# Kernel optimization log

Measured on AMD Instinct MI355X. Metric: run time of the kernel, lower is better.

Reference implementation:

```python
import jax, jax.numpy as jnp
import numpy as np

DROPOUT_RATE = 0.5
CONF_THRESH = 0.85
IGNORE_VALUE = 2
EPS = 1e-07


def setup_inputs() -> dict:
    key = jax.random.key(0)
    k1, k2 = jax.random.split(key)
    B, H, W = 16, 1024, 1024
    pred = jax.random.uniform(k1, (B, H, W), dtype=jnp.float32)
    mask = jax.random.randint(k2, (B, H, W), 0, 3, dtype=jnp.int32)
    return {"pred": pred, "mask": mask}


def _training_need_score(pred, gt, confidence):
    # Higher = needs more training: CW=4, UW=3, UC=2, CC=1 (+/- confidence bonus)
    is_correct = (pred > 0.5) == (gt == 1.0)
    is_conf = confidence > CONF_THRESH
    score = jnp.where(is_conf & is_correct, 1.0,
            jnp.where(~is_conf & is_correct, 2.0,
            jnp.where(~is_conf & ~is_correct, 3.0, 4.0))).astype(pred.dtype)
    bonus = (confidence - 0.5) * 0.5
    return jnp.where(is_correct, score - bonus, score + bonus)


def _dynamic_masks(pred, mask):
    # Vectorized equivalent of the per-batch nonzero/argsort/scatter loop:
    # rank annotated pixels per batch by descending need-score; top n_train -> train.
    B, H, W = mask.shape
    annotated = (mask != IGNORE_VALUE).reshape(B, H * W)
    gt = mask.astype(pred.dtype)
    confidence = jnp.maximum(pred, 1.0 - pred)
    scores = _training_need_score(pred, gt, confidence).reshape(B, H * W)
    neg_inf = jnp.asarray(-jnp.inf, scores.dtype)
    masked_scores = jnp.where(annotated, scores, neg_inf)
    order = jnp.argsort(-masked_scores, axis=1)          # descending score order
    rank = jnp.argsort(order, axis=1)                    # rank of each pixel in that order
    n_points = annotated.sum(axis=1)
    n_train = (n_points.astype(jnp.float32) * (1.0 - DROPOUT_RATE)).astype(jnp.int32)
    train = annotated & (rank < n_train[:, None])
    holdout = annotated & ~train
    return train.reshape(B, H, W), holdout.reshape(B, H, W)


def reference(pred, mask):
    if pred.ndim == 4 and pred.shape[1] == 1:
        pred = pred[:, 0]
    train_mask, holdout_mask = _dynamic_masks(pred, mask)
    gt = mask.astype(pred.dtype)
    p = jnp.clip(pred, EPS, 1.0 - EPS)
    bce = -(gt * jnp.log(p) + (1.0 - gt) * jnp.log(1.0 - p))
    tm = train_mask.astype(pred.dtype)
    loss = (bce * tm).sum() / (tm.sum() + EPS)
    return loss, train_mask, holdout_mask
```

## Files before the change

kernel.cpp:

```cpp
#include <hip/hip_runtime.h>
#include <stdint.h>

#define NBATCH 16
#define HW_ (1 << 20)
#define TPB 256

#define NBPB_H 32
#define TPB_H 512
#define EPB_H (HW_ / NBPB_H)
#define ITER_H (EPB_H / (TPB_H * 4))

#define NBINS 8192
#define FBASE 0x3F400

#define NBPB_F 256
#define FCHUNK (HW_ / NBPB_F)

#define CAND_CAP 32768
#define LCAP 512
#define TIE_CAP 4096
#define CNT_STRIDE 64

typedef float f4v __attribute__((ext_vector_type(4)));

struct BParams {
    unsigned int k;
    unsigned int bin1f;
    unsigned int r;
    unsigned int mode;
};

__device__ __forceinline__ unsigned int score_bits(float p, int m) {
    bool correct = (p > 0.5f) == (m == 1);
    float conf = fmaxf(p, 1.0f - p);
    float base = correct ? ((conf > 0.85f) ? 1.0f : 2.0f)
                         : ((conf > 0.85f) ? 4.0f : 3.0f);
    float bonus = (conf - 0.5f) * 0.5f;
    float s = correct ? (base - bonus) : (base + bonus);
    return __float_as_uint(s);
}

__global__ void k_hist1(const float4* __restrict__ pred4, const int4* __restrict__ mask4,
                        unsigned int* __restrict__ hist1) {
    __shared__ unsigned int lh[NBINS];
    int b = blockIdx.x / NBPB_H;
    int blk = blockIdx.x % NBPB_H;
    for (int i = threadIdx.x; i < NBINS; i += TPB_H) lh[i] = 0;
    __syncthreads();
    int l4base = blk * (EPB_H / 4);
    for (int j = 0; j < ITER_H; j++) {
        int i4l = l4base + j * TPB_H + threadIdx.x;
        size_t g4 = (size_t)b * (HW_ / 4) + i4l;
        float4 p = pred4[g4];
        int4 m = mask4[g4];
        float pa[4] = {p.x, p.y, p.z, p.w};
        int ma[4] = {m.x, m.y, m.z, m.w};
#pragma unroll
        for (int l = 0; l < 4; l++) {
            if (ma[l] != 2) {
                unsigned int sb = score_bits(pa[l], ma[l]);
                int fb = (int)(sb >> 12) - FBASE;
                fb = min(max(fb, 0), NBINS - 1);
                atomicAdd(&lh[fb], 1u);
            }
        }
    }
    __syncthreads();
    for (int i = threadIdx.x; i < NBINS; i += TPB_H)
        if (lh[i]) atomicAdd(&hist1[b * NBINS + i], lh[i]);
}

__global__ void k_find1(const unsigned int* __restrict__ hist1, BParams* prm) {
    int b = blockIdx.x;
    int t = threadIdx.x;
    __shared__ unsigned int cs_[257];
    const unsigned int* h = hist1 + (size_t)b * NBINS;
    {
        const uint4* h4 = (const uint4*)(h + t * 32);
        unsigned int s = 0;
#pragma unroll
        for (int j = 0; j < 8; j++) { uint4 v = h4[j]; s += v.x + v.y + v.z + v.w; }
        cs_[t] = s;
        if (t == 0) cs_[256] = 0;
    }
    __syncthreads();
    for (int off = 1; off < 256; off <<= 1) {
        unsigned int a = (t + off < 256) ? cs_[t + off] : 0u;
        __syncthreads();
        cs_[t] += a;
        __syncthreads();
    }
    unsigned int n = cs_[0];
    unsigned int k = (unsigned int)(int)((float)n * 0.5f);
    if (k == 0) {
        if (t == 0) {
            BParams P;
            P.k = 0; P.bin1f = 0xFFFFFFFFu; P.r = 0; P.mode = 0;
            prm[b] = P;
        }
        return;
    }
    if (cs_[t] >= k && cs_[t + 1] < k) {
        unsigned int cum = cs_[t + 1];
        for (int j = 31; j >= 0; j--) {
            unsigned int hb = h[t * 32 + j];
            if (cum + hb >= k) {
                BParams P;
                P.k = k;
                P.bin1f = (unsigned int)(FBASE + t * 32 + j);
                P.r = k - cum;
                P.mode = 1;
                prm[b] = P;
                break;
            }
            cum += hb;
        }
    }
}

__global__ void k_main(const float4* __restrict__ pred4, const int4* __restrict__ mask4,
                       const BParams* __restrict__ prm, float* __restrict__ out,
                       float* __restrict__ partials, unsigned int* __restrict__ cand_cnt,
                       unsigned int* __restrict__ cand_idx, unsigned int* __restrict__ cand_sb,
                       float* __restrict__ cand_bce) {
    int b = blockIdx.x / NBPB_F;
    int blk = blockIdx.x % NBPB_F;
    BParams P = prm[b];
    unsigned int target = P.bin1f;
    __shared__ unsigned int lcode[FCHUNK / 4];
    __shared__ float red[TPB];
    __shared__ unsigned int l_idx[LCAP];
    __shared__ unsigned int l_sb[LCAP];
    __shared__ float l_bce[LCAP];
    __shared__ unsigned int lcnt;
    __shared__ unsigned int gbase;
    if (threadIdx.x == 0) lcnt = 0;
    __syncthreads();
    float acc = 0.0f;
    int ibase = blk * FCHUNK;
    for (int j = 0; j < FCHUNK / (TPB * 4); j++) {
        int v = j * TPB + threadIdx.x;
        size_t g4 = (size_t)b * (HW_ / 4) + (ibase / 4) + v;
        float4 p = pred4[g4];
        int4 m = mask4[g4];
        float pa[4] = {p.x, p.y, p.z, p.w};
        int ma[4] = {m.x, m.y, m.z, m.w};
        unsigned int cw = 0;
#pragma unroll
        for (int l = 0; l < 4; l++) {
            bool ann = (ma[l] != 2);
            unsigned int sb = score_bits(pa[l], ma[l]);
            unsigned int fine = sb >> 12;
            bool tr = ann && (fine > target);
            bool amb = ann && (fine == target);
            unsigned int code = (tr ? 1u : 0u) | ((ann && !tr) ? 2u : 0u);
            cw |= code << (8 * l);
            float bce = 0.0f;
            if (tr || amb) {
                float pc = fminf(fmaxf(pa[l], 1e-7f), 1.0f - 1e-7f);
                bce = (ma[l] == 1) ? -__logf(pc) : -__logf(1.0f - pc);
            }
            if (tr) acc += bce;
            if (amb) {
                unsigned int p0 = atomicAdd(&lcnt, 1u);
                if (p0 < LCAP) {
                    l_idx[p0] = (unsigned int)(ibase + v * 4 + l);
                    l_sb[p0] = sb;
                    l_bce[p0] = bce;
                } else {
                    unsigned int gp = atomicAdd(&cand_cnt[b * CNT_STRIDE], 1u);
                    if (gp < CAND_CAP) {
                        size_t o = (size_t)b * CAND_CAP + gp;
                        cand_idx[o] = (unsigned int)(ibase + v * 4 + l);
                        cand_sb[o] = sb;
                        cand_bce[o] = bce;
                    }
                }
            }
        }
        lcode[v] = cw;
    }
    __syncthreads();
    unsigned int n = min(lcnt, (unsigned int)LCAP);
    if (threadIdx.x == 0 && n > 0)
        gbase = atomicAdd(&cand_cnt[b * CNT_STRIDE], n);
    __syncthreads();
    for (unsigned int i = threadIdx.x; i < n; i += TPB) {
        unsigned int pos = gbase + i;
        if (pos < CAND_CAP) {
            size_t o = (size_t)b * CAND_CAP + pos;
            cand_idx[o] = l_idx[i];
            cand_sb[o] = l_sb[i];
            cand_bce[o] = l_bce[i];
        }
    }
    float* trout = out + 1;
    float* hoout = out + 1 + (size_t)NBATCH * HW_;
    size_t Gbase = (size_t)b * HW_ + (size_t)ibase;
    for (int v = threadIdx.x; v < FCHUNK / 4 - 1; v += TPB) {
        unsigned int w0 = lcode[v];
        unsigned int w1 = lcode[v + 1];
        unsigned int c0 = (w0 >> 24) & 0xFFu;
        unsigned int c1 = w1 & 0xFFu;
        unsigned int c2 = (w1 >> 8) & 0xFFu;
        unsigned int c3 = (w1 >> 16) & 0xFFu;
        int e = 3 + 4 * v;
        f4v tv = { (float)(c0 & 1u), (float)(c1 & 1u), (float)(c2 & 1u), (float)(c3 & 1u) };
        f4v hv = { (float)((c0 >> 1) & 1u), (float)((c1 >> 1) & 1u),
                   (float)((c2 >> 1) & 1u), (float)((c3 >> 1) & 1u) };
        __builtin_nontemporal_store(tv, (f4v*)(trout + Gbase + e));
        __builtin_nontemporal_store(hv, (f4v*)(hoout + Gbase + e));
    }
    if (threadIdx.x < 3) {
        unsigned int c = (lcode[0] >> (8 * threadIdx.x)) & 0xFFu;
        trout[Gbase + threadIdx.x] = (float)(c & 1u);
        hoout[Gbase + threadIdx.x] = (float)((c >> 1) & 1u);
    }
    if (threadIdx.x == 3) {
        unsigned int c = (lcode[FCHUNK / 4 - 1] >> 24) & 0xFFu;
        trout[Gbase + FCHUNK - 1] = (float)(c & 1u);
        hoout[Gbase + FCHUNK - 1] = (float)((c >> 1) & 1u);
    }
    red[threadIdx.x] = acc;
    __syncthreads();
    for (int off = TPB / 2; off > 0; off >>= 1) {
        if (threadIdx.x < off) red[threadIdx.x] += red[threadIdx.x + off];
        __syncthreads();
    }
    if (threadIdx.x == 0) partials[blockIdx.x] = red[0];
}

__global__ void k_fixup(const unsigned int* __restrict__ cand_cnt,
                        const unsigned int* __restrict__ cand_idx,
                        const unsigned int* __restrict__ cand_sb,
                        const float* __restrict__ cand_bce,
                        const BParams* __restrict__ prm, float* __restrict__ out,
                        float* __restrict__ tie_partials) {
    int b = blockIdx.x;
    int t = threadIdx.x;
    __shared__ unsigned int h[4096];
    __shared__ unsigned int cs_[257];
    __shared__ unsigned int tie_idx[TIE_CAP];
    __shared__ unsigned int misc[8];
    __shared__ float red[TPB];
    BParams P = prm[b];
    if (P.mode == 0) {
        if (t == 0) tie_partials[b] = 0.0f;
        return;
    }
    unsigned int C = cand_cnt[b * CNT_STRIDE];
    if (C > CAND_CAP) C = CAND_CAP;
    const unsigned int* ci = cand_idx + (size_t)b * CAND_CAP;
    const unsigned int* cs = cand_sb + (size_t)b * CAND_CAP;
    const float* cb = cand_bce + (size_t)b * CAND_CAP;
    for (int i = t; i < 4096; i += TPB) h[i] = 0;
    if (t < 8) misc[t] = (t == 4) ? 0xFFFFFFFFu : 0u;
    __syncthreads();
    for (unsigned int i = t; i < C; i += TPB)
        atomicAdd(&h[cs[i] & 0xFFFu], 1u);
    __syncthreads();
    {
        unsigned int gs = 0;
#pragma unroll
        for (int j = 0; j < 16; j++) gs += h[t * 16 + j];
        cs_[t] = gs;
        if (t == 0) cs_[256] = 0;
    }
    __syncthreads();
    for (int off = 1; off < 256; off <<= 1) {
        unsigned int a = (t + off < 256) ? cs_[t + off] : 0u;
        __syncthreads();
        cs_[t] += a;
        __syncthreads();
    }
    if (cs_[t] >= P.r && cs_[t + 1] < P.r) {
        unsigned int cum = cs_[t + 1];
        for (int j = 15; j >= 0; j--) {
            unsigned int hb = h[t * 16 + j];
            if (cum + hb >= P.r) {
                unsigned int T = P.r - cum;
                misc[0] = (unsigned int)(t * 16 + j);
                misc[1] = T;
                misc[2] = (T == hb) ? 1u : 0u;
                break;
            }
            cum += hb;
        }
    }
    __syncthreads();
    unsigned int vstar = misc[0], T = misc[1];
    bool allTies = (misc[2] != 0);
    unsigned int idxcut;
    if (allTies) {
        idxcut = 0xFFFFFFFFu;
    } else {
        for (unsigned int i = t; i < C; i += TPB) {
            if ((cs[i] & 0xFFFu) == vstar) {
                unsigned int p = atomicAdd(&misc[3], 1u);
                if (p < TIE_CAP) tie_idx[p] = ci[i];
            }
        }
        __syncthreads();
        unsigned int E2 = misc[3];
        if (E2 > TIE_CAP) E2 = TIE_CAP;
        for (unsigned int i = t; i < E2; i += TPB) {
            unsigned int vi = tie_idx[i];
            unsigned int cnt = 0;
            for (unsigned int j = 0; j < E2; j++) cnt += (tie_idx[j] < vi) ? 1u : 0u;
            if (cnt == T - 1) misc[4] = vi;
        }
        __syncthreads();
        idxcut = misc[4];
    }
    float acc = 0.0f;
    float* trout = out + 1;
    float* hoout = out + 1 + (size_t)NBATCH * HW_;
    size_t base = (size_t)b * HW_;
    for (unsigned int i = t; i < C; i += TPB) {
        unsigned int low = cs[i] & 0xFFFu;
        bool tr = (low > vstar) || (low == vstar && ci[i] <= idxcut);
        if (tr) {
            trout[base + ci[i]] = 1.0f;
            hoout[base + ci[i]] = 0.0f;
            acc += cb[i];
        }
    }
    red[t] = acc;
    __syncthreads();
    for (int off = TPB / 2; off > 0; off >>= 1) {
        if (t < off) red[t] += red[t + off];
        __syncthreads();
    }
    if (t == 0) tie_partials[b] = red[0];
}

__global__ void k_loss(const float* __restrict__ partials, const float* __restrict__ tie_partials,
                       const BParams* __restrict__ prm, float* __restrict__ out) {
    __shared__ double red[TPB];
    double s = 0.0;
    for (int i = threadIdx.x; i < NBATCH * NBPB_F; i += TPB) s += (double)partials[i];
    if (threadIdx.x < NBATCH) s += (double)tie_partials[threadIdx.x];
    red[threadIdx.x] = s;
    __syncthreads();
    for (int off = TPB / 2; off > 0; off >>= 1) {
        if (threadIdx.x < off) red[threadIdx.x] += red[threadIdx.x + off];
        __syncthreads();
    }
    if (threadIdx.x == 0) {
        unsigned long long den = 0;
        for (int b = 0; b < NBATCH; b++) den += prm[b].k;
        float denf = (float)den + 1e-7f;
        out[0] = (float)red[0] / denf;
    }
}

extern "C" void kernel_launch(void* const* d_in, const int* in_sizes, int n_in,
                              void* d_out, int out_size, void* d_ws, size_t ws_size,
                              hipStream_t stream) {
    const float4* pred4 = (const float4*)d_in[0];
    const int4* mask4 = (const int4*)d_in[1];
    float* out = (float*)d_out;

    unsigned int* hist1 = (unsigned int*)d_ws;
    unsigned int* cand_cnt = hist1 + NBATCH * NBINS;
    BParams* prm = (BParams*)(cand_cnt + NBATCH * CNT_STRIDE);
    float* partials = (float*)(prm + NBATCH);
    float* tie_partials = partials + NBATCH * NBPB_F;
    unsigned int* cand_idx = (unsigned int*)(tie_partials + NBATCH);
    unsigned int* cand_sb = cand_idx + NBATCH * CAND_CAP;
    float* cand_bce = (float*)(cand_sb + NBATCH * CAND_CAP);

    size_t zero_bytes = (size_t)(NBATCH * NBINS + NBATCH * CNT_STRIDE) * 4;
    hipMemsetAsync(d_ws, 0, zero_bytes, stream);

    k_hist1<<<dim3(NBATCH * NBPB_H), dim3(TPB_H), 0, stream>>>(pred4, mask4, hist1);
    k_find1<<<dim3(NBATCH), dim3(TPB), 0, stream>>>(hist1, prm);
    k_main<<<dim3(NBATCH * NBPB_F), dim3(TPB), 0, stream>>>(pred4, mask4, prm, out, partials,
                                                            cand_cnt, cand_idx, cand_sb, cand_bce);
    k_fixup<<<dim3(NBATCH), dim3(TPB), 0, stream>>>(cand_cnt, cand_idx, cand_sb, cand_bce,
                                                    prm, out, tie_partials);
    k_loss<<<dim3(1), dim3(TPB), 0, stream>>>(partials, tie_partials, prm, out);
}
```

Before: 284.2 us.

## Fuse all five stages into one cooperative persistent kernel with grid syncs

Replaces the histogram, threshold-find, main, fixup and loss kernels with a single cooperative kernel of 1024 blocks that separates the stages with grid.sync(), reusing one shared-memory union across phases. Each block handles the same input chunk in both the histogram and main passes, which may give L2 reuse of pred/mask on the second read, and it removes four kernel launch gaps. The cost is grid-wide barriers, one fixed block count (occupancy limited by a 32KB histogram per block plus the union), and serial phases where only 16 blocks work while the rest wait. TIE_CAP is also reduced.

```diff
diff --git a/kernel.cpp b/kernel.cpp
--- a/kernel.cpp
+++ b/kernel.cpp
@@ -1,24 +1,24 @@
 #include <hip/hip_runtime.h>
+#include <hip/hip_cooperative_groups.h>
 #include <stdint.h>
+
+namespace cg = cooperative_groups;
 
 #define NBATCH 16
 #define HW_ (1 << 20)
 #define TPB 256
-
-#define NBPB_H 32
-#define TPB_H 512
-#define EPB_H (HW_ / NBPB_H)
-#define ITER_H (EPB_H / (TPB_H * 4))
+#define NBLOCKS 1024
+#define BPB (NBLOCKS / NBATCH)
+#define EPB (HW_ / BPB)
+#define E4PB (EPB / 4)
+#define ITERS (E4PB / TPB)
 
 #define NBINS 8192
 #define FBASE 0x3F400
 
-#define NBPB_F 256
-#define FCHUNK (HW_ / NBPB_F)
-
 #define CAND_CAP 32768
 #define LCAP 512
-#define TIE_CAP 4096
+#define TIE_CAP 1024
 #define CNT_STRIDE 64
 
 typedef float f4v __attribute__((ext_vector_type(4)));
@@ -29,6 +29,22 @@
     unsigned int r;
     unsigned int mode;
 };
+
+struct SP1 { unsigned int hist[NBINS]; };
+struct SP2 { unsigned int cs_[257]; };
+struct SP3 {
+    unsigned int lcode[E4PB];
+    unsigned int l_idx[LCAP]; unsigned int l_sb[LCAP]; float l_bce[LCAP];
+    float red[TPB];
+    unsigned int lcnt, gbase;
+};
+struct SP4 {
+    unsigned int h[4096]; unsigned int cs_[257];
+    unsigned int tie_idx[TIE_CAP]; unsigned int misc[8];
+    float red[TPB];
+};
+struct SP5 { double red[TPB]; };
+union SmemU { SP1 p1; SP2 p2; SP3 p3; SP4 p4; SP5 p5; };
 
 __device__ __forceinline__ unsigned int score_bits(float p, int m) {
     bool correct = (p > 0.5f) == (m == 1);
@@ -40,19 +56,29 @@
     return __float_as_uint(s);
 }
 
-__global__ void k_hist1(const float4* __restrict__ pred4, const int4* __restrict__ mask4,
-                        unsigned int* __restrict__ hist1) {
-    __shared__ unsigned int lh[NBINS];
-    int b = blockIdx.x / NBPB_H;
-    int blk = blockIdx.x % NBPB_H;
-    for (int i = threadIdx.x; i < NBINS; i += TPB_H) lh[i] = 0;
+__global__ __launch_bounds__(TPB, 4) void k_all(
+    const float4* __restrict__ pred4, const int4* __restrict__ mask4,
+    float* __restrict__ out,
+    unsigned int* __restrict__ hist1, unsigned int* __restrict__ cand_cnt,
+    BParams* __restrict__ prm, float* __restrict__ partials,
+    float* __restrict__ tie_partials,
+    unsigned int* __restrict__ cand_idx, unsigned int* __restrict__ cand_sb,
+    float* __restrict__ cand_bce)
+{
+    cg::grid_group grid = cg::this_grid();
+    __shared__ SmemU sm;
+    const int b = blockIdx.x / BPB;
+    const int blk = blockIdx.x % BPB;
+    const int t = threadIdx.x;
+    const size_t batch4 = (size_t)b * (HW_ / 4);
+    const int l4base = blk * E4PB;
+
+    for (int i = t; i < NBINS; i += TPB) sm.p1.hist[i] = 0;
     __syncthreads();
-    int l4base = blk * (EPB_H / 4);
-    for (int j = 0; j < ITER_H; j++) {
-        int i4l = l4base + j * TPB_H + threadIdx.x;
-        size_t g4 = (size_t)b * (HW_ / 4) + i4l;
-        float4 p = pred4[g4];
-        int4 m = mask4[g4];
+    for (int j = 0; j < ITERS; j++) {
+        int i4 = l4base + j * TPB + t;
+        float4 p = pred4[batch4 + i4];
+        int4 m = mask4[batch4 + i4];
         float pa[4] = {p.x, p.y, p.z, p.w};
         int ma[4] = {m.x, m.y, m.z, m.w};
 #pragma unroll
@@ -61,296 +87,268 @@
                 unsigned int sb = score_bits(pa[l], ma[l]);
                 int fb = (int)(sb >> 12) - FBASE;
                 fb = min(max(fb, 0), NBINS - 1);
-                atomicAdd(&lh[fb], 1u);
+                atomicAdd(&sm.p1.hist[fb], 1u);
             }
         }
     }
     __syncthreads();
-    for (int i = threadIdx.x; i < NBINS; i += TPB_H)
-        if (lh[i]) atomicAdd(&hist1[b * NBINS + i], lh[i]);
-}
-
-__global__ void k_find1(const unsigned int* __restrict__ hist1, BParams* prm) {
-    int b = blockIdx.x;
-    int t = threadIdx.x;
-    __shared__ unsigned int cs_[257];
-    const unsigned int* h = hist1 + (size_t)b * NBINS;
+    for (int i = t; i < NBINS; i += TPB) {
+        unsigned int v = sm.p1.hist[i];
+        if (v) atomicAdd(&hist1[b * NBINS + i], v);
+    }
+    grid.sync();
+
+    if (blockIdx.x < NBATCH) {
+        int bb = blockIdx.x;
+        const unsigned int* h = hist1 + (size_t)bb * NBINS;
+        {
+            const uint4* h4 = (const uint4*)(h + t * 32);
+            unsigned int s = 0;
+#pragma unroll
+            for (int j = 0; j < 8; j++) { uint4 v = h4[j]; s += v.x + v.y + v.z + v.w; }
+            sm.p2.cs_[t] = s;
+            if (t == 0) sm.p2.cs_[256] = 0;
+        }
+        __syncthreads();
+        for (int off = 1; off < 256; off <<= 1) {
+            unsigned int a = (t + off < 256) ? sm.p2.cs_[t + off] : 0u;
+            __syncthreads();
+            sm.p2.cs_[t] += a;
+            __syncthreads();
+        }
+        unsigned int n = sm.p2.cs_[0];
+        unsigned int k = (unsigned int)(int)((float)n * 0.5f);
+        if (k == 0) {
+            if (t == 0) {
+                BParams P; P.k = 0; P.bin1f = 0xFFFFFFFFu; P.r = 0; P.mode = 0;
+                prm[bb] = P;
+            }
+        } else if (sm.p2.cs_[t] >= k && sm.p2.cs_[t + 1] < k) {
+            unsigned int cum = sm.p2.cs_[t + 1];
+            for (int j = 31; j >= 0; j--) {
+                unsigned int hb = h[t * 32 + j];
+                if (cum + hb >= k) {
+                    BParams P;
+                    P.k = k; P.bin1f = (unsigned int)(FBASE + t * 32 + j);
+                    P.r = k - cum; P.mode = 1;
+                    prm[bb] = P;
+                    break;
+                }
+                cum += hb;
+            }
+        }
+    }
+    grid.sync();
+
     {
-        const uint4* h4 = (const uint4*)(h + t * 32);
-        unsigned int s = 0;
+        BParams P = prm[b];
+        unsigned int target = P.bin1f;
+        if (t == 0) sm.p3.lcnt = 0;
+        __syncthreads();
+        float acc = 0.0f;
+        for (int j = 0; j < ITERS; j++) {
+            int v = j * TPB + t;
+            float4 p = pred4[batch4 + l4base + v];
+            int4 m = mask4[batch4 + l4base + v];
+            float pa[4] = {p.x, p.y, p.z, p.w};
+            int ma[4] = {m.x, m.y, m.z, m.w};
+            unsigned int cw = 0;
 #pragma unroll
-        for (int j = 0; j < 8; j++) { uint4 v = h4[j]; s += v.x + v.y + v.z + v.w; }
-        cs_[t] = s;
-        if (t == 0) cs_[256] = 0;
-    }
-    __syncthreads();
-    for (int off = 1; off < 256; off <<= 1) {
-        unsigned int a = (t + off < 256) ? cs_[t + off] : 0u;
-        __syncthreads();
-        cs_[t] += a;
-        __syncthreads();
-    }
-    unsigned int n = cs_[0];
-    unsigned int k = (unsigned int)(int)((float)n * 0.5f);
-    if (k == 0) {
+            for (int l = 0; l < 4; l++) {
+                bool ann = (ma[l] != 2);
+                unsigned int sb = score_bits(pa[l], ma[l]);
+                unsigned int fine = sb >> 12;
+                bool tr = ann && (fine > target);
+                bool amb = ann && (fine == target);
+                unsigned int code = (tr ? 1u : 0u) | ((ann && !tr) ? 2u : 0u);
+                cw |= code << (8 * l);
+                float bce = 0.0f;
+                if (tr || amb) {
+                    float pc = fminf(fmaxf(pa[l], 1e-7f), 1.0f - 1e-7f);
+                    bce = (ma[l] == 1) ? -__logf(pc) : -__logf(1.0f - pc);
+                }
+                if (tr) acc += bce;
+                if (amb) {
+                    unsigned int p0 = atomicAdd(&sm.p3.lcnt, 1u);
+                    if (p0 < LCAP) {
+                        sm.p3.l_idx[p0] = (unsigned int)(blk * EPB + v * 4 + l);
+                        sm.p3.l_sb[p0] = sb;
+                        sm.p3.l_bce[p0] = bce;
+                    } else {
+                        unsigned int gp = atomicAdd(&cand_cnt[b * CNT_STRIDE], 1u);
+                        if (gp < CAND_CAP) {
+                            size_t o = (size_t)b * CAND_CAP + gp;
+                            cand_idx[o] = (unsigned int)(blk * EPB + v * 4 + l);
+                            cand_sb[o] = sb;
+                            cand_bce[o] = bce;
+                        }
+                    }
+                }
+            }
+            sm.p3.lcode[v] = cw;
+        }
+        __syncthreads();
+        unsigned int n = min(sm.p3.lcnt, (unsigned int)LCAP);
+        if (t == 0 && n > 0)
+            sm.p3.gbase = atomicAdd(&cand_cnt[b * CNT_STRIDE], n);
+        __syncthreads();
+        for (unsigned int i = t; i < n; i += TPB) {
+            unsigned int pos = sm.p3.gbase + i;
+            if (pos < CAND_CAP) {
+                size_t o = (size_t)b * CAND_CAP + pos;
+                cand_idx[o] = sm.p3.l_idx[i];
+                cand_sb[o] = sm.p3.l_sb[i];
+                cand_bce[o] = sm.p3.l_bce[i];
+            }
+        }
+        float* trout = out + 1;
+        float* hoout = out + 1 + (size_t)NBATCH * HW_;
+        size_t Gbase = (size_t)b * HW_ + (size_t)blk * EPB;
+        for (int v = t; v < E4PB - 1; v += TPB) {
+            unsigned int w0 = sm.p3.lcode[v];
+            unsigned int w1 = sm.p3.lcode[v + 1];
+            unsigned int c0 = (w0 >> 24) & 0xFFu;
+            unsigned int c1 = w1 & 0xFFu;
+            unsigned int c2 = (w1 >> 8) & 0xFFu;
+            unsigned int c3 = (w1 >> 16) & 0xFFu;
+            int e = 3 + 4 * v;
+            f4v tv = { (float)(c0 & 1u), (float)(c1 & 1u), (float)(c2 & 1u), (float)(c3 & 1u) };
+            f4v hv = { (float)((c0 >> 1) & 1u), (float)((c1 >> 1) & 1u),
+                       (float)((c2 >> 1) & 1u), (float)((c3 >> 1) & 1u) };
+            __builtin_nontemporal_store(tv, (f4v*)(trout + Gbase + e));
+            __builtin_nontemporal_store(hv, (f4v*)(hoout + Gbase + e));
+        }
+        if (t < 3) {
+            unsigned int c = (sm.p3.lcode[0] >> (8 * t)) & 0xFFu;
+            trout[Gbase + t] = (float)(c & 1u);
+            hoout[Gbase + t] = (float)((c >> 1) & 1u);
+        }
+        if (t == 3) {
+            unsigned int c = (sm.p3.lcode[E4PB - 1] >> 24) & 0xFFu;
+            trout[Gbase + EPB - 1] = (float)(c & 1u);
+            hoout[Gbase + EPB - 1] = (float)((c >> 1) & 1u);
+        }
+        sm.p3.red[t] = acc;
+        __syncthreads();
+        for (int off = TPB / 2; off > 0; off >>= 1) {
+            if (t < off) sm.p3.red[t] += sm.p3.red[t + off];
+            __syncthreads();
+        }
+        if (t == 0) partials[blockIdx.x] = sm.p3.red[0];
+    }
+    grid.sync();
+
+    if (blockIdx.x < NBATCH) {
+        int bb = blockIdx.x;
+        BParams P = prm[bb];
+        if (P.mode == 0) {
+            if (t == 0) tie_partials[bb] = 0.0f;
+        } else {
+            unsigned int C = cand_cnt[bb * CNT_STRIDE];
+            if (C > CAND_CAP) C = CAND_CAP;
+            const unsigned int* ci = cand_idx + (size_t)bb * CAND_CAP;
+            const unsigned int* cs = cand_sb + (size_t)bb * CAND_CAP;
+            const float* cb = cand_bce + (size_t)bb * CAND_CAP;
+            for (int i = t; i < 4096; i += TPB) sm.p4.h[i] = 0;
+            if (t < 8) sm.p4.misc[t] = (t == 4) ? 0xFFFFFFFFu : 0u;
+            __syncthreads();
+            for (unsigned int i = t; i < C; i += TPB)
+                atomicAdd(&sm.p4.h[cs[i] & 0xFFFu], 1u);
+            __syncthreads();
+            {
+                unsigned int gs = 0;
+#pragma unroll
+                for (int j = 0; j < 16; j++) gs += sm.p4.h[t * 16 + j];
+                sm.p4.cs_[t] = gs;
+                if (t == 0) sm.p4.cs_[256] = 0;
+            }
+            __syncthreads();
+            for (int off = 1; off < 256; off <<= 1) {
+                unsigned int a = (t + off < 256) ? sm.p4.cs_[t + off] : 0u;
+                __syncthreads();
+                sm.p4.cs_[t] += a;
+                __syncthreads();
+            }
+            if (sm.p4.cs_[t] >= P.r && sm.p4.cs_[t + 1] < P.r) {
+                unsigned int cum = sm.p4.cs_[t + 1];
+                for (int j = 15; j >= 0; j--) {
+                    unsigned int hb = sm.p4.h[t * 16 + j];
+                    if (cum + hb >= P.r) {
+                        unsigned int T = P.r - cum;
+                        sm.p4.misc[0] = (unsigned int)(t * 16 + j);
+                        sm.p4.misc[1] = T;
+                        sm.p4.misc[2] = (T == hb) ? 1u : 0u;
+                        break;
+                    }
+                    cum += hb;
+                }
+            }
+            __syncthreads();
+            unsigned int vstar = sm.p4.misc[0], T = sm.p4.misc[1];
+            bool allTies = (sm.p4.misc[2] != 0);
+            unsigned int idxcut;
+            if (allTies) {
+                idxcut = 0xFFFFFFFFu;
+            } else {
+                for (unsigned int i = t; i < C; i += TPB) {
+                    if ((cs[i] & 0xFFFu) == vstar) {
+                        unsigned int p = atomicAdd(&sm.p4.misc[3], 1u);
+                        if (p < TIE_CAP) sm.p4.tie_idx[p] = ci[i];
+                    }
+                }
+                __syncthreads();
+                unsigned int E2 = sm.p4.misc[3];
+                if (E2 > TIE_CAP) E2 = TIE_CAP;
+                for (unsigned int i = t; i < E2; i += TPB) {
+                    unsigned int vi = sm.p4.tie_idx[i];
+                    unsigned int cnt = 0;
+                    for (unsigned int j = 0; j < E2; j++)
+                        cnt += (sm.p4.tie_idx[j] < vi) ? 1u : 0u;
+                    if (cnt == T - 1) sm.p4.misc[4] = vi;
+                }
+                __syncthreads();
+                idxcut = sm.p4.misc[4];
+            }
+            float acc = 0.0f;
+            float* trout = out + 1;
+            float* hoout = out + 1 + (size_t)NBATCH * HW_;
+            size_t base = (size_t)bb * HW_;
+            for (unsigned int i = t; i < C; i += TPB) {
+                unsigned int low = cs[i] & 0xFFFu;
+                bool tr = (low > vstar) || (low == vstar && ci[i] <= idxcut);
+                if (tr) {
+                    trout[base + ci[i]] = 1.0f;
+                    hoout[base + ci[i]] = 0.0f;
+                    acc += cb[i];
+                }
+            }
+            sm.p4.red[t] = acc;
+            __syncthreads();
+            for (int off = TPB / 2; off > 0; off >>= 1) {
+                if (t < off) sm.p4.red[t] += sm.p4.red[t + off];
+                __syncthreads();
+            }
+            if (t == 0) tie_partials[bb] = sm.p4.red[0];
+        }
+    }
+    grid.sync();
+
+    if (blockIdx.x == 0) {
+        double s = 0.0;
+        for (int i = t; i < NBLOCKS; i += TPB) s += (double)partials[i];
+        if (t < NBATCH) s += (double)tie_partials[t];
+        sm.p5.red[t] = s;
+        __syncthreads();
+        for (int off = TPB / 2; off > 0; off >>= 1) {
+            if (t < off) sm.p5.red[t] += sm.p5.red[t + off];
+            __syncthreads();
+        }
         if (t == 0) {
-            BParams P;
-            P.k = 0; P.bin1f = 0xFFFFFFFFu; P.r = 0; P.mode = 0;
-            prm[b] = P;
-        }
-        return;
-    }
-    if (cs_[t] >= k && cs_[t + 1] < k) {
-        unsigned int cum = cs_[t + 1];
-        for (int j = 31; j >= 0; j--) {
-            unsigned int hb = h[t * 32 + j];
-            if (cum + hb >= k) {
-                BParams P;
-                P.k = k;
-                P.bin1f = (unsigned int)(FBASE + t * 32 + j);
-                P.r = k - cum;
-                P.mode = 1;
-                prm[b] = P;
-                break;
-            }
-            cum += hb;
-        }
-    }
-}
-
-__global__ void k_main(const float4* __restrict__ pred4, const int4* __restrict__ mask4,
-                       const BParams* __restrict__ prm, float* __restrict__ out,
-                       float* __restrict__ partials, unsigned int* __restrict__ cand_cnt,
-                       unsigned int* __restrict__ cand_idx, unsigned int* __restrict__ cand_sb,
-                       float* __restrict__ cand_bce) {
-    int b = blockIdx.x / NBPB_F;
-    int blk = blockIdx.x % NBPB_F;
-    BParams P = prm[b];
-    unsigned int target = P.bin1f;
-    __shared__ unsigned int lcode[FCHUNK / 4];
-    __shared__ float red[TPB];
-    __shared__ unsigned int l_idx[LCAP];
-    __shared__ unsigned int l_sb[LCAP];
-    __shared__ float l_bce[LCAP];
-    __shared__ unsigned int lcnt;
-    __shared__ unsigned int gbase;
-    if (threadIdx.x == 0) lcnt = 0;
-    __syncthreads();
-    float acc = 0.0f;
-    int ibase = blk * FCHUNK;
-    for (int j = 0; j < FCHUNK / (TPB * 4); j++) {
-        int v = j * TPB + threadIdx.x;
-        size_t g4 = (size_t)b * (HW_ / 4) + (ibase / 4) + v;
-        float4 p = pred4[g4];
-        int4 m = mask4[g4];
-        float pa[4] = {p.x, p.y, p.z, p.w};
-        int ma[4] = {m.x, m.y, m.z, m.w};
-        unsigned int cw = 0;
-#pragma unroll
-        for (int l = 0; l < 4; l++) {
-            bool ann = (ma[l] != 2);
-            unsigned int sb = score_bits(pa[l], ma[l]);
-            unsigned int fine = sb >> 12;
-            bool tr = ann && (fine > target);
-            bool amb = ann && (fine == target);
-            unsigned int code = (tr ? 1u : 0u) | ((ann && !tr) ? 2u : 0u);
-            cw |= code << (8 * l);
-            float bce = 0.0f;
-            if (tr || amb) {
-                float pc = fminf(fmaxf(pa[l], 1e-7f), 1.0f - 1e-7f);
-                bce = (ma[l] == 1) ? -__logf(pc) : -__logf(1.0f - pc);
-            }
-            if (tr) acc += bce;
-            if (amb) {
-                unsigned int p0 = atomicAdd(&lcnt, 1u);
-                if (p0 < LCAP) {
-                    l_idx[p0] = (unsigned int)(ibase + v * 4 + l);
-                    l_sb[p0] = sb;
-                    l_bce[p0] = bce;
-                } else {
-                    unsigned int gp = atomicAdd(&cand_cnt[b * CNT_STRIDE], 1u);
-                    if (gp < CAND_CAP) {
-                        size_t o = (size_t)b * CAND_CAP + gp;
-                        cand_idx[o] = (unsigned int)(ibase + v * 4 + l);
-                        cand_sb[o] = sb;
-                        cand_bce[o] = bce;
-                    }
-                }
-            }
-        }
-        lcode[v] = cw;
-    }
-    __syncthreads();
-    unsigned int n = min(lcnt, (unsigned int)LCAP);
-    if (threadIdx.x == 0 && n > 0)
-        gbase = atomicAdd(&cand_cnt[b * CNT_STRIDE], n);
-    __syncthreads();
-    for (unsigned int i = threadIdx.x; i < n; i += TPB) {
-        unsigned int pos = gbase + i;
-        if (pos < CAND_CAP) {
-            size_t o = (size_t)b * CAND_CAP + pos;
-            cand_idx[o] = l_idx[i];
-            cand_sb[o] = l_sb[i];
-            cand_bce[o] = l_bce[i];
-        }
-    }
-    float* trout = out + 1;
-    float* hoout = out + 1 + (size_t)NBATCH * HW_;
-    size_t Gbase = (size_t)b * HW_ + (size_t)ibase;
-    for (int v = threadIdx.x; v < FCHUNK / 4 - 1; v += TPB) {
-        unsigned int w0 = lcode[v];
-        unsigned int w1 = lcode[v + 1];
-        unsigned int c0 = (w0 >> 24) & 0xFFu;
-        unsigned int c1 = w1 & 0xFFu;
-        unsigned int c2 = (w1 >> 8) & 0xFFu;
-        unsigned int c3 = (w1 >> 16) & 0xFFu;
-        int e = 3 + 4 * v;
-        f4v tv = { (float)(c0 & 1u), (float)(c1 & 1u), (float)(c2 & 1u), (float)(c3 & 1u) };
-        f4v hv = { (float)((c0 >> 1) & 1u), (float)((c1 >> 1) & 1u),
-                   (float)((c2 >> 1) & 1u), (float)((c3 >> 1) & 1u) };
-        __builtin_nontemporal_store(tv, (f4v*)(trout + Gbase + e));
-        __builtin_nontemporal_store(hv, (f4v*)(hoout + Gbase + e));
-    }
-    if (threadIdx.x < 3) {
-        unsigned int c = (lcode[0] >> (8 * threadIdx.x)) & 0xFFu;
-        trout[Gbase + threadIdx.x] = (float)(c & 1u);
-        hoout[Gbase + threadIdx.x] = (float)((c >> 1) & 1u);
-    }
-    if (threadIdx.x == 3) {
-        unsigned int c = (lcode[FCHUNK / 4 - 1] >> 24) & 0xFFu;
-        trout[Gbase + FCHUNK - 1] = (float)(c & 1u);
-        hoout[Gbase + FCHUNK - 1] = (float)((c >> 1) & 1u);
-    }
-    red[threadIdx.x] = acc;
-    __syncthreads();
-    for (int off = TPB / 2; off > 0; off >>= 1) {
-        if (threadIdx.x < off) red[threadIdx.x] += red[threadIdx.x + off];
-        __syncthreads();
-    }
-    if (threadIdx.x == 0) partials[blockIdx.x] = red[0];
-}
-
-__global__ void k_fixup(const unsigned int* __restrict__ cand_cnt,
-                        const unsigned int* __restrict__ cand_idx,
-                        const unsigned int* __restrict__ cand_sb,
-                        const float* __restrict__ cand_bce,
-                        const BParams* __restrict__ prm, float* __restrict__ out,
-                        float* __restrict__ tie_partials) {
-    int b = blockIdx.x;
-    int t = threadIdx.x;
-    __shared__ unsigned int h[4096];
-    __shared__ unsigned int cs_[257];
-    __shared__ unsigned int tie_idx[TIE_CAP];
-    __shared__ unsigned int misc[8];
-    __shared__ float red[TPB];
-    BParams P = prm[b];
-    if (P.mode == 0) {
-        if (t == 0) tie_partials[b] = 0.0f;
-        return;
-    }
-    unsigned int C = cand_cnt[b * CNT_STRIDE];
-    if (C > CAND_CAP) C = CAND_CAP;
-    const unsigned int* ci = cand_idx + (size_t)b * CAND_CAP;
-    const unsigned int* cs = cand_sb + (size_t)b * CAND_CAP;
-    const float* cb = cand_bce + (size_t)b * CAND_CAP;
-    for (int i = t; i < 4096; i += TPB) h[i] = 0;
-    if (t < 8) misc[t] = (t == 4) ? 0xFFFFFFFFu : 0u;
-    __syncthreads();
-    for (unsigned int i = t; i < C; i += TPB)
-        atomicAdd(&h[cs[i] & 0xFFFu], 1u);
-    __syncthreads();
-    {
-        unsigned int gs = 0;
-#pragma unroll
-        for (int j = 0; j < 16; j++) gs += h[t * 16 + j];
-        cs_[t] = gs;
-        if (t == 0) cs_[256] = 0;
-    }
-    __syncthreads();
-    for (int off = 1; off < 256; off <<= 1) {
-        unsigned int a = (t + off < 256) ? cs_[t + off] : 0u;
-        __syncthreads();
-        cs_[t] += a;
-        __syncthreads();
-    }
-    if (cs_[t] >= P.r && cs_[t + 1] < P.r) {
-        unsigned int cum = cs_[t + 1];
-        for (int j = 15; j >= 0; j--) {
-            unsigned int hb = h[t * 16 + j];
-            if (cum + hb >= P.r) {
-                unsigned int T = P.r - cum;
-                misc[0] = (unsigned int)(t * 16 + j);
-                misc[1] = T;
-                misc[2] = (T == hb) ? 1u : 0u;
-                break;
-            }
-            cum += hb;
-        }
-    }
-    __syncthreads();
-    unsigned int vstar = misc[0], T = misc[1];
-    bool allTies = (misc[2] != 0);
-    unsigned int idxcut;
-    if (allTies) {
-        idxcut = 0xFFFFFFFFu;
-    } else {
-        for (unsigned int i = t; i < C; i += TPB) {
-            if ((cs[i] & 0xFFFu) == vstar) {
-                unsigned int p = atomicAdd(&misc[3], 1u);
-                if (p < TIE_CAP) tie_idx[p] = ci[i];
-            }
-        }
-        __syncthreads();
-        unsigned int E2 = misc[3];
-        if (E2 > TIE_CAP) E2 = TIE_CAP;
-        for (unsigned int i = t; i < E2; i += TPB) {
-            unsigned int vi = tie_idx[i];
-            unsigned int cnt = 0;
-            for (unsigned int j = 0; j < E2; j++) cnt += (tie_idx[j] < vi) ? 1u : 0u;
-            if (cnt == T - 1) misc[4] = vi;
-        }
-        __syncthreads();
-        idxcut = misc[4];
-    }
-    float acc = 0.0f;
-    float* trout = out + 1;
-    float* hoout = out + 1 + (size_t)NBATCH * HW_;
-    size_t base = (size_t)b * HW_;
-    for (unsigned int i = t; i < C; i += TPB) {
-        unsigned int low = cs[i] & 0xFFFu;
-        bool tr = (low > vstar) || (low == vstar && ci[i] <= idxcut);
-        if (tr) {
-            trout[base + ci[i]] = 1.0f;
-            hoout[base + ci[i]] = 0.0f;
-            acc += cb[i];
-        }
-    }
-    red[t] = acc;
-    __syncthreads();
-    for (int off = TPB / 2; off > 0; off >>= 1) {
-        if (t < off) red[t] += red[t + off];
-        __syncthreads();
-    }
-    if (t == 0) tie_partials[b] = red[0];
-}
-
-__global__ void k_loss(const float* __restrict__ partials, const float* __restrict__ tie_partials,
-                       const BParams* __restrict__ prm, float* __restrict__ out) {
-    __shared__ double red[TPB];
-    double s = 0.0;
-    for (int i = threadIdx.x; i < NBATCH * NBPB_F; i += TPB) s += (double)partials[i];
-    if (threadIdx.x < NBATCH) s += (double)tie_partials[threadIdx.x];
-    red[threadIdx.x] = s;
-    __syncthreads();
-    for (int off = TPB / 2; off > 0; off >>= 1) {
-        if (threadIdx.x < off) red[threadIdx.x] += red[threadIdx.x + off];
-        __syncthreads();
-    }
-    if (threadIdx.x == 0) {
-        unsigned long long den = 0;
-        for (int b = 0; b < NBATCH; b++) den += prm[b].k;
-        float denf = (float)den + 1e-7f;
-        out[0] = (float)red[0] / denf;
+            unsigned long long den = 0;
+            for (int b2 = 0; b2 < NBATCH; b2++) den += prm[b2].k;
+            float denf = (float)den + 1e-7f;
+            out[0] = (float)sm.p5.red[0] / denf;
+        }
     }
 }
 
@@ -365,7 +363,7 @@
     unsigned int* cand_cnt = hist1 + NBATCH * NBINS;
     BParams* prm = (BParams*)(cand_cnt + NBATCH * CNT_STRIDE);
     float* partials = (float*)(prm + NBATCH);
-    float* tie_partials = partials + NBATCH * NBPB_F;
+    float* tie_partials = partials + NBLOCKS;
     unsigned int* cand_idx = (unsigned int*)(tie_partials + NBATCH);
     unsigned int* cand_sb = cand_idx + NBATCH * CAND_CAP;
     float* cand_bce = (float*)(cand_sb + NBATCH * CAND_CAP);
@@ -373,11 +371,9 @@
     size_t zero_bytes = (size_t)(NBATCH * NBINS + NBATCH * CNT_STRIDE) * 4;
     hipMemsetAsync(d_ws, 0, zero_bytes, stream);
 
-    k_hist1<<<dim3(NBATCH * NBPB_H), dim3(TPB_H), 0, stream>>>(pred4, mask4, hist1);
-    k_find1<<<dim3(NBATCH), dim3(TPB), 0, stream>>>(hist1, prm);
-    k_main<<<dim3(NBATCH * NBPB_F), dim3(TPB), 0, stream>>>(pred4, mask4, prm, out, partials,
-                                                            cand_cnt, cand_idx, cand_sb, cand_bce);
-    k_fixup<<<dim3(NBATCH), dim3(TPB), 0, stream>>>(cand_cnt, cand_idx, cand_sb, cand_bce,
-                                                    prm, out, tie_partials);
-    k_loss<<<dim3(1), dim3(TPB), 0, stream>>>(partials, tie_partials, prm, out);
+    void* args[] = { (void*)&pred4, (void*)&mask4, (void*)&out, (void*)&hist1,
+                     (void*)&cand_cnt, (void*)&prm, (void*)&partials,
+                     (void*)&tie_partials, (void*)&cand_idx, (void*)&cand_sb,
+                     (void*)&cand_bce };
+    hipLaunchCooperativeKernel((void*)k_all, dim3(NBLOCKS), dim3(TPB), args, 0, stream);
 }
```

Measured after the change: 716.6 us. +152.2%, slower.
